# Kernel optimization log

Hardware: AMD Instinct MI355X
Metric: run time of the kernel (lower is better)

## Reference

```python
import jax, jax.numpy as jnp
import numpy as np

N_PTS = 131072
K_POSE = 4
J = 24
P_NUM = 64
R_COMP = 32
POSE_DIM = 32
GRID = (512, 512, 128)
MAT_MODE = ((0, 1), (0, 2), (1, 2))


def sample_line(line, xs):
    # line: [k, R, G], xs: [N] in [-1, 1].
    # Equivalent to F.grid_sample on a [k,R,G,1] map with grid x-coord fixed to 0
    # (W==1 so the x dim is degenerate) -> 1D linear interpolation along G.
    G = line.shape[-1]
    pos = (xs + 1.0) * 0.5 * (G - 1)
    i0 = jnp.clip(jnp.floor(pos), 0, G - 1).astype(jnp.int32)
    i1 = jnp.clip(i0 + 1, 0, G - 1)
    w = pos - i0.astype(xs.dtype)
    v0 = jnp.take(line, i0, axis=-1)  # [k,R,N]
    v1 = jnp.take(line, i1, axis=-1)
    return v0 * (1.0 - w) + v1 * w


def blend(w, A):
    # w: [1,N,J], A: [1,J,4,4] -> per-point blended LBS transform [1,N,4,4]
    return jnp.einsum('bnj,bjuv->bnuv', w, A)


def lbs_points(pts, T, inverse):
    Rm = T[..., :3, :3]
    t = T[..., :3, 3]
    if inverse:
        return jnp.einsum('bnij,bnj->bni', jnp.linalg.inv(Rm), pts - t)
    return jnp.einsum('bnij,bnj->bni', Rm, pts) + t


def lbs_dirs(d, T, inverse):
    Rm = T[..., :3, :3]
    if inverse:
        return jnp.einsum('bnij,bnj->bni', jnp.linalg.inv(Rm), d)
    return jnp.einsum('bnij,bnj->bni', Rm, d)


def setup_inputs() -> dict:
    key = jax.random.key(0)
    ks = jax.random.split(key, 12)
    pose_pts = 0.3 * jax.random.normal(ks[0], (1, N_PTS, 3), jnp.float32)
    pose_dirs = jax.random.normal(ks[1], (1, N_PTS, 3), jnp.float32)
    sw = jax.random.uniform(ks[2], (1, N_PTS, J), dtype=jnp.float32)
    skinning_weight = sw / jnp.sum(sw, axis=-1, keepdims=True)
    eye = jnp.eye(4, dtype=jnp.float32)
    A = eye + 0.2 * jax.random.normal(ks[3], (1, J, 4, 4), jnp.float32)
    big_A = eye + 0.2 * jax.random.normal(ks[4], (1, J, 4, 4), jnp.float32)
    tbounds = jnp.array([[-1.5, -1.5, -1.5], [1.5, 1.5, 1.5]], jnp.float32)
    coord_line0 = 0.1 * jax.random.normal(ks[5], (P_NUM, R_COMP, GRID[0], 1), jnp.float32)
    coord_line1 = 0.1 * jax.random.normal(ks[6], (P_NUM, R_COMP, GRID[1], 1), jnp.float32)
    coord_line2 = 0.1 * jax.random.normal(ks[7], (P_NUM, R_COMP, GRID[2], 1), jnp.float32)
    feat_line0 = 0.1 * jax.random.normal(ks[8], (P_NUM, R_COMP, POSE_DIM, 1), jnp.float32)
    feat_line1 = 0.1 * jax.random.normal(ks[9], (P_NUM, R_COMP, POSE_DIM, 1), jnp.float32)
    feat_line2 = 0.1 * jax.random.normal(ks[10], (P_NUM, R_COMP, POSE_DIM, 1), jnp.float32)
    tw = jax.random.uniform(ks[11], (K_POSE,), dtype=jnp.float32) + 0.1
    topk_weight = tw / jnp.sum(tw)  # L1-normalized top-k pose weights
    topk_id = jax.random.randint(jax.random.fold_in(key, 7), (K_POSE,), 0, P_NUM, dtype=jnp.int32)
    return dict(pose_pts=pose_pts, pose_dirs=pose_dirs, skinning_weight=skinning_weight,
                A=A, big_A=big_A, tbounds=tbounds,
                coord_line0=coord_line0, coord_line1=coord_line1, coord_line2=coord_line2,
                feat_line0=feat_line0, feat_line1=feat_line1, feat_line2=feat_line2,
                topk_weight=topk_weight, topk_id=topk_id)


def reference(pose_pts, pose_dirs, skinning_weight, A, big_A, tbounds,
              coord_line0, coord_line1, coord_line2,
              feat_line0, feat_line1, feat_line2,
              topk_weight, topk_id):
    # --- backward_deform: observed pose -> t-pose (inv A) -> big/canonical pose (big_A) ---
    T_A = blend(skinning_weight, A)
    T_big = blend(skinning_weight, big_A)
    tpose = lbs_points(pose_pts, T_A, inverse=True)
    cnl_pts = lbs_points(tpose, T_big, inverse=False)   # [1,N,3]
    tdirs = lbs_dirs(pose_dirs, T_A, inverse=True)
    cnl_dirs = lbs_dirs(tdirs, T_big, inverse=False)    # [1,N,3]
    # --- get_pose_feat: normalize_pts detaches pts, then TensoRF-style line sampling ---
    npts = jax.lax.stop_gradient(cnl_pts)
    npts = (npts - tbounds[0]) / (tbounds[1] - tbounds[0]) * 2.0 - 1.0  # [1,N,3]
    coord_lines = (coord_line0, coord_line1, coord_line2)
    feat_lines = (feat_line0, feat_line1, feat_line2)
    coords, feats = [], []
    for i in range(3):
        line = coord_lines[i][topk_id][..., 0]           # [k,R,G_i]
        coords.append(sample_line(line, npts[0, :, i]))  # [k,R,N]
        feats.append(feat_lines[i][topk_id][..., 0])     # [k,R,C]
    planes = []
    for p, (i0, i1) in enumerate(MAT_MODE):
        t = coords[i0] * coords[i1]                      # [k,R,N] outer-product term
        planes.append(jnp.einsum('krn,krc->knc', t, feats[p]))  # reduce over R
    pose_feats = jnp.concatenate(planes, axis=-1)        # [k,N,3C]
    pose_feat = jnp.sum(topk_weight[:, None, None] * pose_feats, axis=0, keepdims=True)
    return jnp.concatenate([cnl_pts, cnl_dirs, pose_feat], axis=-1)  # [1,N,102]
```

## Files before the change

### kernel.cpp

```cpp
#include <hip/hip_runtime.h>

#define NPTS 131072
#define G0 512
#define G1 512
#define G2 128

typedef float v4f __attribute__((ext_vector_type(4)));
typedef __attribute__((ext_vector_type(8))) short short8;

__device__ float g_linesT[4*(G0+G1+G2)*32];
__device__ unsigned short g_featB[3*4*2*64*8];

__device__ __forceinline__ unsigned short bf16rne(float x){
  unsigned int u = __float_as_uint(x);
  u += 0x7fffu + ((u >> 16) & 1u);
  return (unsigned short)(u >> 16);
}

__global__ void prep_lines(const float* __restrict__ c0,
                           const float* __restrict__ c1,
                           const float* __restrict__ c2,
                           const int* __restrict__ topk_id) {
  int e = blockIdx.x*blockDim.x + threadIdx.x;
  const int T0 = 4*G0*32, T1 = 4*G1*32, T2 = 4*G2*32;
  if (e >= T0+T1+T2) return;
  const float* src; int G; int e2 = e;
  if (e2 < T0)            { src = c0; G = G0; }
  else if (e2 < T0+T1)    { e2 -= T0; src = c1; G = G1; }
  else                    { e2 -= T0+T1; src = c2; G = G2; }
  int kk  = e2 / (G*32);
  int rem = e2 - kk*G*32;
  int g = rem >> 5;
  int r = rem & 31;
  int id = topk_id[kk];
  g_linesT[e] = src[(id*32 + r)*G + g];
}

__global__ void prep_featB(const float* __restrict__ f0,
                           const float* __restrict__ f1,
                           const float* __restrict__ f2,
                           const float* __restrict__ tw,
                           const int* __restrict__ topk_id) {
  int e = blockIdx.x*blockDim.x + threadIdx.x;
  if (e >= 3*4*2*64*8) return;
  int j    =  e        & 7;
  int lane = (e >> 3)  & 63;
  int tcol = (e >> 9)  & 1;
  int s    = (e >> 10) & 3;
  int p    =  e >> 12;
  int r = ((lane >> 4) << 3) + j;
  int c = tcol*16 + (lane & 15);
  const float* f = (p == 0) ? f0 : ((p == 1) ? f1 : f2);
  float v = tw[s] * f[(topk_id[s]*32 + r)*32 + c];
  g_featB[e] = bf16rne(v);
}

__global__ __launch_bounds__(256) void fuse_main(
    const float* __restrict__ pts, const float* __restrict__ dirs,
    const float* __restrict__ sw,  const float* __restrict__ Am,
    const float* __restrict__ Bm,  const float* __restrict__ tb,
    float* __restrict__ out)
{
  __shared__ float sA[384];
  __shared__ float sB[384];
  __shared__ unsigned short sFeat[3*4*2*64*8];
  __shared__ int   sI0[3][256];
  __shared__ int   sI1[3][256];
  __shared__ float sWw[3][256];

  const int tid = threadIdx.x;

  for (int i = tid; i < 384; i += 256){ sA[i] = Am[i]; sB[i] = Bm[i]; }
  {
    const uint4* gs = reinterpret_cast<const uint4*>(g_featB);
    uint4* gd = reinterpret_cast<uint4*>(sFeat);
    for (int i = tid; i < (3*4*2*64*8)/8; i += 256) gd[i] = gs[i];
  }
  __syncthreads();

  const int n = blockIdx.x*256 + tid;
  float swv[24];
  {
    const float4* swp = reinterpret_cast<const float4*>(sw + n*24);
    #pragma unroll
    for (int i = 0; i < 6; i++){
      float4 v = swp[i];
      swv[4*i] = v.x; swv[4*i+1] = v.y; swv[4*i+2] = v.z; swv[4*i+3] = v.w;
    }
  }
  float RA[9] = {0,0,0,0,0,0,0,0,0}, tA[3] = {0,0,0};
  float RB[9] = {0,0,0,0,0,0,0,0,0}, tB[3] = {0,0,0};
  #pragma unroll
  for (int j = 0; j < 24; j++){
    float w = swv[j];
    const float* a = sA + j*16;
    const float* b = sB + j*16;
    RA[0] = fmaf(w, a[0], RA[0]); RA[1] = fmaf(w, a[1], RA[1]); RA[2] = fmaf(w, a[2], RA[2]); tA[0] = fmaf(w, a[3],  tA[0]);
    RA[3] = fmaf(w, a[4], RA[3]); RA[4] = fmaf(w, a[5], RA[4]); RA[5] = fmaf(w, a[6], RA[5]); tA[1] = fmaf(w, a[7],  tA[1]);
    RA[6] = fmaf(w, a[8], RA[6]); RA[7] = fmaf(w, a[9], RA[7]); RA[8] = fmaf(w, a[10],RA[8]); tA[2] = fmaf(w, a[11], tA[2]);
    RB[0] = fmaf(w, b[0], RB[0]); RB[1] = fmaf(w, b[1], RB[1]); RB[2] = fmaf(w, b[2], RB[2]); tB[0] = fmaf(w, b[3],  tB[0]);
    RB[3] = fmaf(w, b[4], RB[3]); RB[4] = fmaf(w, b[5], RB[4]); RB[5] = fmaf(w, b[6], RB[5]); tB[1] = fmaf(w, b[7],  tB[1]);
    RB[6] = fmaf(w, b[8], RB[6]); RB[7] = fmaf(w, b[9], RB[7]); RB[8] = fmaf(w, b[10],RB[8]); tB[2] = fmaf(w, b[11], tB[2]);
  }
  float c00 = RA[4]*RA[8] - RA[5]*RA[7];
  float c01 = RA[5]*RA[6] - RA[3]*RA[8];
  float c02 = RA[3]*RA[7] - RA[4]*RA[6];
  float det = RA[0]*c00 + RA[1]*c01 + RA[2]*c02;
  float idet = 1.0f/det;
  float i00 = c00*idet;
  float i01 = (RA[2]*RA[7] - RA[1]*RA[8])*idet;
  float i02 = (RA[1]*RA[5] - RA[2]*RA[4])*idet;
  float i10 = c01*idet;
  float i11 = (RA[0]*RA[8] - RA[2]*RA[6])*idet;
  float i12 = (RA[2]*RA[3] - RA[0]*RA[5])*idet;
  float i20 = c02*idet;
  float i21 = (RA[1]*RA[6] - RA[0]*RA[7])*idet;
  float i22 = (RA[0]*RA[4] - RA[1]*RA[3])*idet;

  float px = pts[n*3+0], py = pts[n*3+1], pz = pts[n*3+2];
  float dx = dirs[n*3+0], dy = dirs[n*3+1], dz = dirs[n*3+2];
  float qx = px - tA[0], qy = py - tA[1], qz = pz - tA[2];
  float tpx = i00*qx + i01*qy + i02*qz;
  float tpy = i10*qx + i11*qy + i12*qz;
  float tpz = i20*qx + i21*qy + i22*qz;
  float cx = RB[0]*tpx + RB[1]*tpy + RB[2]*tpz + tB[0];
  float cy = RB[3]*tpx + RB[4]*tpy + RB[5]*tpz + tB[1];
  float cz = RB[6]*tpx + RB[7]*tpy + RB[8]*tpz + tB[2];
  float tdx = i00*dx + i01*dy + i02*dz;
  float tdy = i10*dx + i11*dy + i12*dz;
  float tdz = i20*dx + i21*dy + i22*dz;
  float cdx = RB[0]*tdx + RB[1]*tdy + RB[2]*tdz;
  float cdy = RB[3]*tdx + RB[4]*tdy + RB[5]*tdz;
  float cdz = RB[6]*tdx + RB[7]*tdy + RB[8]*tdz;

  {
    float* o = out + (size_t)n*102;
    o[0] = cx; o[1] = cy; o[2] = cz; o[3] = cdx; o[4] = cdy; o[5] = cdz;
  }

  {
    float lo0 = tb[0], lo1 = tb[1], lo2 = tb[2];
    float hi0 = tb[3], hi1 = tb[4], hi2 = tb[5];
    float xs[3]; int Gs[3] = {G0, G1, G2};
    xs[0] = (cx - lo0)/(hi0 - lo0)*2.0f - 1.0f;
    xs[1] = (cy - lo1)/(hi1 - lo1)*2.0f - 1.0f;
    xs[2] = (cz - lo2)/(hi2 - lo2)*2.0f - 1.0f;
    #pragma unroll
    for (int a = 0; a < 3; a++){
      float pos = (xs[a] + 1.0f)*0.5f*(float)(Gs[a]-1);
      float fi = floorf(pos);
      fi = fminf(fmaxf(fi, 0.0f), (float)(Gs[a]-1));
      int i0 = (int)fi;
      int i1 = min(i0 + 1, Gs[a]-1);
      float w = pos - (float)i0;
      sI0[a][tid] = i0; sI1[a][tid] = i1; sWw[a][tid] = w;
    }
  }
  __syncthreads();

  const int lane = tid & 63;
  const int wv   = tid >> 6;
  const int m    = lane & 15;
  const int q    = lane >> 4;
  const float* lt0 = g_linesT;
  const float* lt1 = g_linesT + 4*G0*32;
  const float* lt2 = g_linesT + 4*(G0+G1)*32;
  const short8* fb = reinterpret_cast<const short8*>(sFeat);

  for (int t = 0; t < 4; t++){
    const int pl = wv*64 + t*16 + m;
    const int a0i0 = sI0[0][pl], a0i1 = sI1[0][pl];
    const int a1i0 = sI0[1][pl], a1i1 = sI1[1][pl];
    const int a2i0 = sI0[2][pl], a2i1 = sI1[2][pl];
    const float w0 = sWw[0][pl], w1 = sWw[1][pl], w2 = sWw[2][pl];
    v4f acc00 = {0,0,0,0}, acc01 = {0,0,0,0};
    v4f acc10 = {0,0,0,0}, acc11 = {0,0,0,0};
    v4f acc20 = {0,0,0,0}, acc21 = {0,0,0,0};
    #pragma unroll
    for (int s = 0; s < 4; s++){
      float c0[8], c1[8], c2[8];
      {
        const float* p0 = lt0 + (s*G0 + a0i0)*32 + q*8;
        const float* p1 = lt0 + (s*G0 + a0i1)*32 + q*8;
        float4 v0a = *(const float4*)p0, v0b = *(const float4*)(p0+4);
        float4 v1a = *(const float4*)p1, v1b = *(const float4*)(p1+4);
        c0[0] = fmaf(w0, v1a.x - v0a.x, v0a.x);
        c0[1] = fmaf(w0, v1a.y - v0a.y, v0a.y);
        c0[2] = fmaf(w0, v1a.z - v0a.z, v0a.z);
        c0[3] = fmaf(w0, v1a.w - v0a.w, v0a.w);
        c0[4] = fmaf(w0, v1b.x - v0b.x, v0b.x);
        c0[5] = fmaf(w0, v1b.y - v0b.y, v0b.y);
        c0[6] = fmaf(w0, v1b.z - v0b.z, v0b.z);
        c0[7] = fmaf(w0, v1b.w - v0b.w, v0b.w);
      }
      {
        const float* p0 = lt1 + (s*G1 + a1i0)*32 + q*8;
        const float* p1 = lt1 + (s*G1 + a1i1)*32 + q*8;
        float4 v0a = *(const float4*)p0, v0b = *(const float4*)(p0+4);
        float4 v1a = *(const float4*)p1, v1b = *(const float4*)(p1+4);
        c1[0] = fmaf(w1, v1a.x - v0a.x, v0a.x);
        c1[1] = fmaf(w1, v1a.y - v0a.y, v0a.y);
        c1[2] = fmaf(w1, v1a.z - v0a.z, v0a.z);
        c1[3] = fmaf(w1, v1a.w - v0a.w, v0a.w);
        c1[4] = fmaf(w1, v1b.x - v0b.x, v0b.x);
        c1[5] = fmaf(w1, v1b.y - v0b.y, v0b.y);
        c1[6] = fmaf(w1, v1b.z - v0b.z, v0b.z);
        c1[7] = fmaf(w1, v1b.w - v0b.w, v0b.w);
      }
      {
        const float* p0 = lt2 + (s*G2 + a2i0)*32 + q*8;
        const float* p1 = lt2 + (s*G2 + a2i1)*32 + q*8;
        float4 v0a = *(const float4*)p0, v0b = *(const float4*)(p0+4);
        float4 v1a = *(const float4*)p1, v1b = *(const float4*)(p1+4);
        c2[0] = fmaf(w2, v1a.x - v0a.x, v0a.x);
        c2[1] = fmaf(w2, v1a.y - v0a.y, v0a.y);
        c2[2] = fmaf(w2, v1a.z - v0a.z, v0a.z);
        c2[3] = fmaf(w2, v1a.w - v0a.w, v0a.w);
        c2[4] = fmaf(w2, v1b.x - v0b.x, v0b.x);
        c2[5] = fmaf(w2, v1b.y - v0b.y, v0b.y);
        c2[6] = fmaf(w2, v1b.z - v0b.z, v0b.z);
        c2[7] = fmaf(w2, v1b.w - v0b.w, v0b.w);
      }
      short8 A0, A1, A2;
      #pragma unroll
      for (int j = 0; j < 8; j++){
        A0[j] = (short)bf16rne(c0[j]*c1[j]);
        A1[j] = (short)bf16rne(c0[j]*c2[j]);
        A2[j] = (short)bf16rne(c1[j]*c2[j]);
      }
      short8 B00 = fb[(0*8 + s*2 + 0)*64 + lane];
      short8 B01 = fb[(0*8 + s*2 + 1)*64 + lane];
      short8 B10 = fb[(1*8 + s*2 + 0)*64 + lane];
      short8 B11 = fb[(1*8 + s*2 + 1)*64 + lane];
      short8 B20 = fb[(2*8 + s*2 + 0)*64 + lane];
      short8 B21 = fb[(2*8 + s*2 + 1)*64 + lane];
      acc00 = __builtin_amdgcn_mfma_f32_16x16x32_bf16(A0, B00, acc00, 0, 0, 0);
      acc01 = __builtin_amdgcn_mfma_f32_16x16x32_bf16(A0, B01, acc01, 0, 0, 0);
      acc10 = __builtin_amdgcn_mfma_f32_16x16x32_bf16(A1, B10, acc10, 0, 0, 0);
      acc11 = __builtin_amdgcn_mfma_f32_16x16x32_bf16(A1, B11, acc11, 0, 0, 0);
      acc20 = __builtin_amdgcn_mfma_f32_16x16x32_bf16(A2, B20, acc20, 0, 0, 0);
      acc21 = __builtin_amdgcn_mfma_f32_16x16x32_bf16(A2, B21, acc21, 0, 0, 0);
    }
    const int rowBase = blockIdx.x*256 + wv*64 + t*16 + q*4;
    #pragma unroll
    for (int v = 0; v < 4; v++){
      float* o = out + (size_t)(rowBase + v)*102 + 6 + m;
      o[0]  = acc00[v];
      o[16] = acc01[v];
      o[32] = acc10[v];
      o[48] = acc11[v];
      o[64] = acc20[v];
      o[80] = acc21[v];
    }
  }
}

extern "C" void kernel_launch(void* const* d_in, const int* in_sizes, int n_in,
                              void* d_out, int out_size, void* d_ws, size_t ws_size,
                              hipStream_t stream) {
  const float* pose_pts  = (const float*)d_in[0];
  const float* pose_dirs = (const float*)d_in[1];
  const float* sw        = (const float*)d_in[2];
  const float* Am        = (const float*)d_in[3];
  const float* Bm        = (const float*)d_in[4];
  const float* tb        = (const float*)d_in[5];
  const float* cl0       = (const float*)d_in[6];
  const float* cl1       = (const float*)d_in[7];
  const float* cl2       = (const float*)d_in[8];
  const float* fl0       = (const float*)d_in[9];
  const float* fl1       = (const float*)d_in[10];
  const float* fl2       = (const float*)d_in[11];
  const float* tw        = (const float*)d_in[12];
  const int*   tkid      = (const int*)d_in[13];
  float* out = (float*)d_out;

  hipLaunchKernelGGL(prep_lines, dim3((4*(G0+G1+G2)*32 + 255)/256), dim3(256), 0, stream,
                     cl0, cl1, cl2, tkid);
  hipLaunchKernelGGL(prep_featB, dim3((3*4*2*64*8 + 255)/256), dim3(256), 0, stream,
                     fl0, fl1, fl2, tw, tkid);
  hipLaunchKernelGGL(fuse_main, dim3(NPTS/256), dim3(256), 0, stream,
                     pose_pts, pose_dirs, sw, Am, Bm, tb, out);
}
```

Baseline: 161.8 us.

## Split skinning and MFMA einsum into separate kernels, merge prep into skin kernel

Folds the line-transpose and feature-prep work into the skinning kernel as extra blocks, so three launches become two. The skinning stage now writes normalized grid positions to a global buffer. A separate MFMA kernel handles one 16-point tile per wave over many more blocks, reading features from global memory instead of copying them to LDS. The goal is more parallelism and occupancy for the gather-plus-MFMA stage and fewer launches. The cost is an extra global round trip for the positions and uncached global feature loads. The transpose write pattern also changes so that source reads are coalesced.

```diff
diff --git a/kernel.cpp b/kernel.cpp
--- a/kernel.cpp
+++ b/kernel.cpp
@@ -5,11 +5,16 @@
 #define G1 512
 #define G2 128
 
+#define SKIN_BLOCKS  512
+#define TRANS_BLOCKS 576
+#define FEAT_BLOCKS  48
+
 typedef float v4f __attribute__((ext_vector_type(4)));
 typedef __attribute__((ext_vector_type(8))) short short8;
 
-__device__ float g_linesT[4*(G0+G1+G2)*32];
+__device__ float  g_linesT[4*(G0+G1+G2)*32];
 __device__ unsigned short g_featB[3*4*2*64*8];
+__device__ float4 g_pos[NPTS];
 
 __device__ __forceinline__ unsigned short bf16rne(float x){
   unsigned int u = __float_as_uint(x);
@@ -17,68 +22,59 @@
   return (unsigned short)(u >> 16);
 }
 
-__global__ void prep_lines(const float* __restrict__ c0,
-                           const float* __restrict__ c1,
-                           const float* __restrict__ c2,
-                           const int* __restrict__ topk_id) {
-  int e = blockIdx.x*blockDim.x + threadIdx.x;
-  const int T0 = 4*G0*32, T1 = 4*G1*32, T2 = 4*G2*32;
-  if (e >= T0+T1+T2) return;
-  const float* src; int G; int e2 = e;
-  if (e2 < T0)            { src = c0; G = G0; }
-  else if (e2 < T0+T1)    { e2 -= T0; src = c1; G = G1; }
-  else                    { e2 -= T0+T1; src = c2; G = G2; }
-  int kk  = e2 / (G*32);
-  int rem = e2 - kk*G*32;
-  int g = rem >> 5;
-  int r = rem & 31;
-  int id = topk_id[kk];
-  g_linesT[e] = src[(id*32 + r)*G + g];
-}
-
-__global__ void prep_featB(const float* __restrict__ f0,
-                           const float* __restrict__ f1,
-                           const float* __restrict__ f2,
-                           const float* __restrict__ tw,
-                           const int* __restrict__ topk_id) {
-  int e = blockIdx.x*blockDim.x + threadIdx.x;
-  if (e >= 3*4*2*64*8) return;
-  int j    =  e        & 7;
-  int lane = (e >> 3)  & 63;
-  int tcol = (e >> 9)  & 1;
-  int s    = (e >> 10) & 3;
-  int p    =  e >> 12;
-  int r = ((lane >> 4) << 3) + j;
-  int c = tcol*16 + (lane & 15);
-  const float* f = (p == 0) ? f0 : ((p == 1) ? f1 : f2);
-  float v = tw[s] * f[(topk_id[s]*32 + r)*32 + c];
-  g_featB[e] = bf16rne(v);
-}
-
-__global__ __launch_bounds__(256) void fuse_main(
+__global__ __launch_bounds__(256) void prep_skin(
     const float* __restrict__ pts, const float* __restrict__ dirs,
     const float* __restrict__ sw,  const float* __restrict__ Am,
     const float* __restrict__ Bm,  const float* __restrict__ tb,
+    const float* __restrict__ c0,  const float* __restrict__ c1,
+    const float* __restrict__ c2,  const float* __restrict__ f0,
+    const float* __restrict__ f1,  const float* __restrict__ f2,
+    const float* __restrict__ tw,  const int* __restrict__ topk_id,
     float* __restrict__ out)
 {
+  const int bid = blockIdx.x;
+  const int tid = threadIdx.x;
+
+  if (bid >= SKIN_BLOCKS) {
+    int pb = bid - SKIN_BLOCKS;
+    if (pb < TRANS_BLOCKS) {
+      int e = pb*256 + tid;
+      const float* src; int logG, outoff;
+      if (e < 65536)       { src = c0; logG = 9; outoff = 0; }
+      else if (e < 131072) { e -= 65536;  src = c1; logG = 9; outoff = 4*G0*32; }
+      else                 { e -= 131072; src = c2; logG = 7; outoff = 4*(G0+G1)*32; }
+      const int G = 1 << logG;
+      int g  = e & (G-1);
+      int t  = e >> logG;
+      int r  = t & 31;
+      int kk = t >> 5;
+      int id = topk_id[kk];
+      float v = src[(id*32 + r)*G + g];
+      g_linesT[outoff + (kk*G + g)*32 + r] = v;
+    } else {
+      int e = (pb - TRANS_BLOCKS)*256 + tid;
+      if (e < 3*4*2*64*8) {
+        int j    =  e        & 7;
+        int lane = (e >> 3)  & 63;
+        int tcol = (e >> 9)  & 1;
+        int s    = (e >> 10) & 3;
+        int p    =  e >> 12;
+        int r = ((lane >> 4) << 3) + j;
+        int cc = tcol*16 + (lane & 15);
+        const float* f = (p == 0) ? f0 : ((p == 1) ? f1 : f2);
+        float v = tw[s] * f[(topk_id[s]*32 + r)*32 + cc];
+        g_featB[e] = bf16rne(v);
+      }
+    }
+    return;
+  }
+
   __shared__ float sA[384];
   __shared__ float sB[384];
-  __shared__ unsigned short sFeat[3*4*2*64*8];
-  __shared__ int   sI0[3][256];
-  __shared__ int   sI1[3][256];
-  __shared__ float sWw[3][256];
-
-  const int tid = threadIdx.x;
-
   for (int i = tid; i < 384; i += 256){ sA[i] = Am[i]; sB[i] = Bm[i]; }
-  {
-    const uint4* gs = reinterpret_cast<const uint4*>(g_featB);
-    uint4* gd = reinterpret_cast<uint4*>(sFeat);
-    for (int i = tid; i < (3*4*2*64*8)/8; i += 256) gd[i] = gs[i];
-  }
   __syncthreads();
 
-  const int n = blockIdx.x*256 + tid;
+  const int n = bid*256 + tid;
   float swv[24];
   {
     const float4* swp = reinterpret_cast<const float4*>(sw + n*24);
@@ -137,121 +133,124 @@
     float* o = out + (size_t)n*102;
     o[0] = cx; o[1] = cy; o[2] = cz; o[3] = cdx; o[4] = cdy; o[5] = cdz;
   }
-
   {
     float lo0 = tb[0], lo1 = tb[1], lo2 = tb[2];
     float hi0 = tb[3], hi1 = tb[4], hi2 = tb[5];
-    float xs[3]; int Gs[3] = {G0, G1, G2};
-    xs[0] = (cx - lo0)/(hi0 - lo0)*2.0f - 1.0f;
-    xs[1] = (cy - lo1)/(hi1 - lo1)*2.0f - 1.0f;
-    xs[2] = (cz - lo2)/(hi2 - lo2)*2.0f - 1.0f;
-    #pragma unroll
-    for (int a = 0; a < 3; a++){
-      float pos = (xs[a] + 1.0f)*0.5f*(float)(Gs[a]-1);
-      float fi = floorf(pos);
-      fi = fminf(fmaxf(fi, 0.0f), (float)(Gs[a]-1));
-      int i0 = (int)fi;
-      int i1 = min(i0 + 1, Gs[a]-1);
-      float w = pos - (float)i0;
-      sI0[a][tid] = i0; sI1[a][tid] = i1; sWw[a][tid] = w;
-    }
-  }
-  __syncthreads();
-
+    float x0 = (cx - lo0)/(hi0 - lo0)*2.0f - 1.0f;
+    float x1 = (cy - lo1)/(hi1 - lo1)*2.0f - 1.0f;
+    float x2 = (cz - lo2)/(hi2 - lo2)*2.0f - 1.0f;
+    float4 p;
+    p.x = (x0 + 1.0f)*0.5f*(float)(G0-1);
+    p.y = (x1 + 1.0f)*0.5f*(float)(G1-1);
+    p.z = (x2 + 1.0f)*0.5f*(float)(G2-1);
+    p.w = 0.0f;
+    g_pos[n] = p;
+  }
+}
+
+__global__ __launch_bounds__(256, 4) void einsum_mfma(float* __restrict__ out)
+{
+  const int tid  = threadIdx.x;
   const int lane = tid & 63;
   const int wv   = tid >> 6;
   const int m    = lane & 15;
   const int q    = lane >> 4;
+  const int tile = blockIdx.x*4 + wv;
+  const int pl   = tile*16 + m;
+
+  float4 pos = g_pos[pl];
+  float f0i = fminf(fmaxf(floorf(pos.x), 0.0f), (float)(G0-1));
+  int a0i0 = (int)f0i; int a0i1 = min(a0i0+1, G0-1); float w0 = pos.x - f0i;
+  float f1i = fminf(fmaxf(floorf(pos.y), 0.0f), (float)(G1-1));
+  int a1i0 = (int)f1i; int a1i1 = min(a1i0+1, G1-1); float w1 = pos.y - f1i;
+  float f2i = fminf(fmaxf(floorf(pos.z), 0.0f), (float)(G2-1));
+  int a2i0 = (int)f2i; int a2i1 = min(a2i0+1, G2-1); float w2 = pos.z - f2i;
+
   const float* lt0 = g_linesT;
   const float* lt1 = g_linesT + 4*G0*32;
   const float* lt2 = g_linesT + 4*(G0+G1)*32;
-  const short8* fb = reinterpret_cast<const short8*>(sFeat);
-
-  for (int t = 0; t < 4; t++){
-    const int pl = wv*64 + t*16 + m;
-    const int a0i0 = sI0[0][pl], a0i1 = sI1[0][pl];
-    const int a1i0 = sI0[1][pl], a1i1 = sI1[1][pl];
-    const int a2i0 = sI0[2][pl], a2i1 = sI1[2][pl];
-    const float w0 = sWw[0][pl], w1 = sWw[1][pl], w2 = sWw[2][pl];
-    v4f acc00 = {0,0,0,0}, acc01 = {0,0,0,0};
-    v4f acc10 = {0,0,0,0}, acc11 = {0,0,0,0};
-    v4f acc20 = {0,0,0,0}, acc21 = {0,0,0,0};
+  const short8* fb = reinterpret_cast<const short8*>(g_featB);
+
+  v4f acc00 = {0,0,0,0}, acc01 = {0,0,0,0};
+  v4f acc10 = {0,0,0,0}, acc11 = {0,0,0,0};
+  v4f acc20 = {0,0,0,0}, acc21 = {0,0,0,0};
+
+  #pragma unroll
+  for (int s = 0; s < 4; s++){
+    float c0[8], c1[8], c2[8];
+    {
+      const float* p0 = lt0 + (s*G0 + a0i0)*32 + q*8;
+      const float* p1 = lt0 + (s*G0 + a0i1)*32 + q*8;
+      float4 v0a = *(const float4*)p0, v0b = *(const float4*)(p0+4);
+      float4 v1a = *(const float4*)p1, v1b = *(const float4*)(p1+4);
+      c0[0] = fmaf(w0, v1a.x - v0a.x, v0a.x);
+      c0[1] = fmaf(w0, v1a.y - v0a.y, v0a.y);
+      c0[2] = fmaf(w0, v1a.z - v0a.z, v0a.z);
+      c0[3] = fmaf(w0, v1a.w - v0a.w, v0a.w);
+      c0[4] = fmaf(w0, v1b.x - v0b.x, v0b.x);
+      c0[5] = fmaf(w0, v1b.y - v0b.y, v0b.y);
+      c0[6] = fmaf(w0, v1b.z - v0b.z, v0b.z);
+      c0[7] = fmaf(w0, v1b.w - v0b.w, v0b.w);
+    }
+    {
+      const float* p0 = lt1 + (s*G1 + a1i0)*32 + q*8;
+      const float* p1 = lt1 + (s*G1 + a1i1)*32 + q*8;
+      float4 v0a = *(const float4*)p0, v0b = *(const float4*)(p0+4);
+      float4 v1a = *(const float4*)p1, v1b = *(const float4*)(p1+4);
+      c1[0] = fmaf(w1, v1a.x - v0a.x, v0a.x);
+      c1[1] = fmaf(w1, v1a.y - v0a.y, v0a.y);
+      c1[2] = fmaf(w1, v1a.z - v0a.z, v0a.z);
+      c1[3] = fmaf(w1, v1a.w - v0a.w, v0a.w);
+      c1[4] = fmaf(w1, v1b.x - v0b.x, v0b.x);
+      c1[5] = fmaf(w1, v1b.y - v0b.y, v0b.y);
+      c1[6] = fmaf(w1, v1b.z - v0b.z, v0b.z);
+      c1[7] = fmaf(w1, v1b.w - v0b.w, v0b.w);
+    }
+    {
+      const float* p0 = lt2 + (s*G2 + a2i0)*32 + q*8;
+      const float* p1 = lt2 + (s*G2 + a2i1)*32 + q*8;
+      float4 v0a = *(const float4*)p0, v0b = *(const float4*)(p0+4);
+      float4 v1a = *(const float4*)p1, v1b = *(const float4*)(p1+4);
+      c2[0] = fmaf(w2, v1a.x - v0a.x, v0a.x);
+      c2[1] = fmaf(w2, v1a.y - v0a.y, v0a.y);
+      c2[2] = fmaf(w2, v1a.z - v0a.z, v0a.z);
+      c2[3] = fmaf(w2, v1a.w - v0a.w, v0a.w);
+      c2[4] = fmaf(w2, v1b.x - v0b.x, v0b.x);
+      c2[5] = fmaf(w2, v1b.y - v0b.y, v0b.y);
+      c2[6] = fmaf(w2, v1b.z - v0b.z, v0b.z);
+      c2[7] = fmaf(w2, v1b.w - v0b.w, v0b.w);
+    }
+    short8 A0, A1, A2;
     #pragma unroll
-    for (int s = 0; s < 4; s++){
-      float c0[8], c1[8], c2[8];
-      {
-        const float* p0 = lt0 + (s*G0 + a0i0)*32 + q*8;
-        const float* p1 = lt0 + (s*G0 + a0i1)*32 + q*8;
-        float4 v0a = *(const float4*)p0, v0b = *(const float4*)(p0+4);
-        float4 v1a = *(const float4*)p1, v1b = *(const float4*)(p1+4);
-        c0[0] = fmaf(w0, v1a.x - v0a.x, v0a.x);
-        c0[1] = fmaf(w0, v1a.y - v0a.y, v0a.y);
-        c0[2] = fmaf(w0, v1a.z - v0a.z, v0a.z);
-        c0[3] = fmaf(w0, v1a.w - v0a.w, v0a.w);
-        c0[4] = fmaf(w0, v1b.x - v0b.x, v0b.x);
-        c0[5] = fmaf(w0, v1b.y - v0b.y, v0b.y);
-        c0[6] = fmaf(w0, v1b.z - v0b.z, v0b.z);
-        c0[7] = fmaf(w0, v1b.w - v0b.w, v0b.w);
-      }
-      {
-        const float* p0 = lt1 + (s*G1 + a1i0)*32 + q*8;
-        const float* p1 = lt1 + (s*G1 + a1i1)*32 + q*8;
-        float4 v0a = *(const float4*)p0, v0b = *(const float4*)(p0+4);
-        float4 v1a = *(const float4*)p1, v1b = *(const float4*)(p1+4);
-        c1[0] = fmaf(w1, v1a.x - v0a.x, v0a.x);
-        c1[1] = fmaf(w1, v1a.y - v0a.y, v0a.y);
-        c1[2] = fmaf(w1, v1a.z - v0a.z, v0a.z);
-        c1[3] = fmaf(w1, v1a.w - v0a.w, v0a.w);
-        c1[4] = fmaf(w1, v1b.x - v0b.x, v0b.x);
-        c1[5] = fmaf(w1, v1b.y - v0b.y, v0b.y);
-        c1[6] = fmaf(w1, v1b.z - v0b.z, v0b.z);
-        c1[7] = fmaf(w1, v1b.w - v0b.w, v0b.w);
-      }
-      {
-        const float* p0 = lt2 + (s*G2 + a2i0)*32 + q*8;
-        const float* p1 = lt2 + (s*G2 + a2i1)*32 + q*8;
-        float4 v0a = *(const float4*)p0, v0b = *(const float4*)(p0+4);
-        float4 v1a = *(const float4*)p1, v1b = *(const float4*)(p1+4);
-        c2[0] = fmaf(w2, v1a.x - v0a.x, v0a.x);
-        c2[1] = fmaf(w2, v1a.y - v0a.y, v0a.y);
-        c2[2] = fmaf(w2, v1a.z - v0a.z, v0a.z);
-        c2[3] = fmaf(w2, v1a.w - v0a.w, v0a.w);
-        c2[4] = fmaf(w2, v1b.x - v0b.x, v0b.x);
-        c2[5] = fmaf(w2, v1b.y - v0b.y, v0b.y);
-        c2[6] = fmaf(w2, v1b.z - v0b.z, v0b.z);
-        c2[7] = fmaf(w2, v1b.w - v0b.w, v0b.w);
-      }
-      short8 A0, A1, A2;
-      #pragma unroll
-      for (int j = 0; j < 8; j++){
-        A0[j] = (short)bf16rne(c0[j]*c1[j]);
-        A1[j] = (short)bf16rne(c0[j]*c2[j]);
-        A2[j] = (short)bf16rne(c1[j]*c2[j]);
-      }
-      short8 B00 = fb[(0*8 + s*2 + 0)*64 + lane];
-      short8 B01 = fb[(0*8 + s*2 + 1)*64 + lane];
-      short8 B10 = fb[(1*8 + s*2 + 0)*64 + lane];
-      short8 B11 = fb[(1*8 + s*2 + 1)*64 + lane];
-      short8 B20 = fb[(2*8 + s*2 + 0)*64 + lane];
-      short8 B21 = fb[(2*8 + s*2 + 1)*64 + lane];
-      acc00 = __builtin_amdgcn_mfma_f32_16x16x32_bf16(A0, B00, acc00, 0, 0, 0);
-      acc01 = __builtin_amdgcn_mfma_f32_16x16x32_bf16(A0, B01, acc01, 0, 0, 0);
-      acc10 = __builtin_amdgcn_mfma_f32_16x16x32_bf16(A1, B10, acc10, 0, 0, 0);
-      acc11 = __builtin_amdgcn_mfma_f32_16x16x32_bf16(A1, B11, acc11, 0, 0, 0);
-      acc20 = __builtin_amdgcn_mfma_f32_16x16x32_bf16(A2, B20, acc20, 0, 0, 0);
-      acc21 = __builtin_amdgcn_mfma_f32_16x16x32_bf16(A2, B21, acc21, 0, 0, 0);
-    }
-    const int rowBase = blockIdx.x*256 + wv*64 + t*16 + q*4;
-    #pragma unroll
-    for (int v = 0; v < 4; v++){
-      float* o = out + (size_t)(rowBase + v)*102 + 6 + m;
-      o[0]  = acc00[v];
-      o[16] = acc01[v];
-      o[32] = acc10[v];
-      o[48] = acc11[v];
-      o[64] = acc20[v];
-      o[80] = acc21[v];
-    }
+    for (int j = 0; j < 8; j++){
+      A0[j] = (short)bf16rne(c0[j]*c1[j]);
+      A1[j] = (short)bf16rne(c0[j]*c2[j]);
+      A2[j] = (short)bf16rne(c1[j]*c2[j]);
+    }
+    short8 B00 = fb[(0*8 + s*2 + 0)*64 + lane];
+    short8 B01 = fb[(0*8 + s*2 + 1)*64 + lane];
+    short8 B10 = fb[(1*8 + s*2 + 0)*64 + lane];
+    short8 B11 = fb[(1*8 + s*2 + 1)*64 + lane];
+    short8 B20 = fb[(2*8 + s*2 + 0)*64 + lane];
+    short8 B21 = fb[(2*8 + s*2 + 1)*64 + lane];
+    acc00 = __builtin_amdgcn_mfma_f32_16x16x32_bf16(A0, B00, acc00, 0, 0, 0);
+    acc01 = __builtin_amdgcn_mfma_f32_16x16x32_bf16(A0, B01, acc01, 0, 0, 0);
+    acc10 = __builtin_amdgcn_mfma_f32_16x16x32_bf16(A1, B10, acc10, 0, 0, 0);
+    acc11 = __builtin_amdgcn_mfma_f32_16x16x32_bf16(A1, B11, acc11, 0, 0, 0);
+    acc20 = __builtin_amdgcn_mfma_f32_16x16x32_bf16(A2, B20, acc20, 0, 0, 0);
+    acc21 = __builtin_amdgcn_mfma_f32_16x16x32_bf16(A2, B21, acc21, 0, 0, 0);
+  }
+
+  const int rowBase = tile*16 + q*4;
+  #pragma unroll
+  for (int v = 0; v < 4; v++){
+    float* o = out + (size_t)(rowBase + v)*102 + 6 + m;
+    o[0]  = acc00[v];
+    o[16] = acc01[v];
+    o[32] = acc10[v];
+    o[48] = acc11[v];
+    o[64] = acc20[v];
+    o[80] = acc21[v];
   }
 }
 
@@ -274,10 +273,8 @@
   const int*   tkid      = (const int*)d_in[13];
   float* out = (float*)d_out;
 
-  hipLaunchKernelGGL(prep_lines, dim3((4*(G0+G1+G2)*32 + 255)/256), dim3(256), 0, stream,
-                     cl0, cl1, cl2, tkid);
-  hipLaunchKernelGGL(prep_featB, dim3((3*4*2*64*8 + 255)/256), dim3(256), 0, stream,
-                     fl0, fl1, fl2, tw, tkid);
-  hipLaunchKernelGGL(fuse_main, dim3(NPTS/256), dim3(256), 0, stream,
-                     pose_pts, pose_dirs, sw, Am, Bm, tb, out);
-}
+  hipLaunchKernelGGL(prep_skin, dim3(SKIN_BLOCKS + TRANS_BLOCKS + FEAT_BLOCKS), dim3(256), 0, stream,
+                     pose_pts, pose_dirs, sw, Am, Bm, tb,
+                     cl0, cl1, cl2, fl0, fl1, fl2, tw, tkid, out);
+  hipLaunchKernelGGL(einsum_mfma, dim3(NPTS/(4*16)), dim3(256), 0, stream, out);
+}
```

Measured after the change: 163.0 us. About the same (+0.7%).
